# Optimization experiments

Hardware: AMD Instinct MI355X
Metric: run time of the kernel (lower is better)

## Reference

```python
import jax, jax.numpy as jnp
import numpy as np

E = 256  # embed_dim (hardcoded in source module)
H = 4    # n_head
D = E // H
SEQ = 32768


def setup_inputs() -> dict:
    key = jax.random.key(0)
    ks = jax.random.split(key, 5)
    x = jax.random.normal(ks[0], (SEQ, E), dtype=jnp.float32)
    in_proj_weight = jax.random.normal(ks[1], (3 * E, E), dtype=jnp.float32) * (1.0 / np.sqrt(E))
    in_proj_bias = jax.random.normal(ks[2], (3 * E,), dtype=jnp.float32) * 0.02
    out_proj_weight = jax.random.normal(ks[3], (E, E), dtype=jnp.float32) * (1.0 / np.sqrt(E))
    out_proj_bias = jax.random.normal(ks[4], (E,), dtype=jnp.float32) * 0.02
    return {
        "x": x,
        "in_proj_weight": in_proj_weight,
        "in_proj_bias": in_proj_bias,
        "out_proj_weight": out_proj_weight,
        "out_proj_bias": out_proj_bias,
    }


def reference(x, in_proj_weight, in_proj_bias, out_proj_weight, out_proj_bias):
    # QKV projections (q uses only the first token of x: single-query decode attention)
    Wq, Wk, Wv = in_proj_weight[:E], in_proj_weight[E:2 * E], in_proj_weight[2 * E:]
    bq, bk, bv = in_proj_bias[:E], in_proj_bias[E:2 * E], in_proj_bias[2 * E:]
    q = x[:1] @ Wq.T + bq            # [1, E]
    k = x @ Wk.T + bk                # [S, E]
    v = x @ Wv.T + bv                # [S, E]

    qh = q.reshape(H, D)             # [H, D] (single query)
    kh = k.reshape(-1, H, D)         # [S, H, D]
    vh = v.reshape(-1, H, D)         # [S, H, D]

    scale = 1.0 / np.sqrt(D).astype(np.float32)
    scores = jnp.einsum("hd,shd->hs", qh, kh) * scale   # [H, S]
    attn = jax.nn.softmax(scores, axis=-1)                # [H, S]
    ctx = jnp.einsum("hs,shd->hd", attn, vh)             # [H, D]

    out = ctx.reshape(1, E) @ out_proj_weight.T + out_proj_bias  # [1, E]
    return out
```

## Files before the change

kernel.cpp:

```cpp
#include <hip/hip_runtime.h>

#define NBLK 256
#define WS_MP   0
#define WS_LP   1024
#define WS_YV   2048
#define WS_B2   3072
#define WS_KQ   3328
#define WS_C4   4352
#define WS_M2   4416
#define WS_YP   266560
#define WS_CNT  528704

__device__ __forceinline__ float dot4(float4 a, float4 b) {
  return a.x * b.x + a.y * b.y + a.z * b.z + a.w * b.w;
}

__device__ __forceinline__ void set_flag(int* slot, int t) {
  __threadfence();
  __syncthreads();
  if (t == 0) __hip_atomic_store(slot, 1, __ATOMIC_RELEASE, __HIP_MEMORY_SCOPE_AGENT);
}
__device__ __forceinline__ void poll_flags(const int* flags, int n, int t) {
  const int idx = t & (n - 1);
  for (;;) {
    int v = __hip_atomic_load((int*)&flags[idx], __ATOMIC_RELAXED, __HIP_MEMORY_SCOPE_AGENT);
    if (__syncthreads_and(v != 0)) break;
    __builtin_amdgcn_s_sleep(2);
  }
  __threadfence();
}

__device__ __forceinline__ void phaseA_kq(const float* __restrict__ x, const float* __restrict__ W,
                                          const float* __restrict__ inb, float* __restrict__ kq,
                                          float* __restrict__ c4, float* sh, int bid, int t) {
  float* xs = sh;
  float* qls = sh + 256;
  float* red = sh + 320;
  const int lane = t & 63, w = t >> 6;
  const int h = bid >> 2, qt = bid & 3;
  if (t < 256) xs[t] = x[t];
  __syncthreads();
  const float4 xv = *(const float4*)&xs[lane * 4];
#pragma unroll
  for (int k = 0; k < 8; ++k) {
    const int eloc = w * 8 + k;
    const int row = h * 64 + eloc;
    float4 wv = *(const float4*)&W[(size_t)row * 256 + lane * 4];
    float p = dot4(wv, xv);
#pragma unroll
    for (int m = 1; m < 64; m <<= 1) p += __shfl_xor(p, m);
    if (lane == 0) qls[eloc] = p + inb[row];
  }
  __syncthreads();
  const int cl = t & 63, ds = t >> 6;
  float acc = 0.f;
#pragma unroll
  for (int d2 = 0; d2 < 8; ++d2) {
    const int d = ds * 8 + d2;
    acc += W[(size_t)(256 + h * 64 + d) * 256 + qt * 64 + cl] * qls[d];
  }
  red[ds * 64 + cl] = acc;
  __syncthreads();
  if (ds == 0) {
    float s = 0.f;
#pragma unroll
    for (int i = 0; i < 8; ++i) s += red[i * 64 + cl];
    kq[h * 256 + qt * 64 + cl] = s;
  }
  if (qt == 0 && t < 64) {
    float v = qls[t] * inb[256 + h * 64 + t];
#pragma unroll
    for (int m = 1; m < 64; m <<= 1) v += __shfl_xor(v, m);
    if (t == 0) c4[h] = v;
  }
}

__device__ __forceinline__ void phaseM2b(const float* __restrict__ W, const float* __restrict__ Wout,
                                         const float* __restrict__ inb, const float* __restrict__ bout,
                                         float* __restrict__ M2, float* __restrict__ bias2,
                                         float* sh, int b2, int t) {
  float* wout_t = sh;
  const int tile = b2 >> 1, sub = b2 & 1;
  const int h = tile >> 4, e0 = (tile & 15) * 16 + sub * 8;
  {
    const int e = t >> 6, d = t & 63;
    wout_t[e * 64 + d] = Wout[(size_t)(e0 + e) * 256 + h * 64 + d];
  }
  __syncthreads();
  const int c = t & 255, eh = t >> 8;
  float acc[4] = {0.f, 0.f, 0.f, 0.f};
#pragma unroll 8
  for (int d = 0; d < 64; ++d) {
    const float wv = W[(size_t)(512 + h * 64 + d) * 256 + c];
#pragma unroll
    for (int e = 0; e < 4; ++e) acc[e] += wv * wout_t[(eh * 4 + e) * 64 + d];
  }
#pragma unroll
  for (int e = 0; e < 4; ++e)
    M2[(size_t)(e0 + eh * 4 + e) * 1024 + h * 256 + c] = acc[e];
  __syncthreads();
  float* red = sh;
  const int oi = t >> 8, seg = t & 255;
  const int e = 2 * b2 + oi;
  red[oi * 256 + seg] = Wout[(size_t)e * 256 + seg] * inb[512 + seg];
  __syncthreads();
  for (int s = 128; s > 0; s >>= 1) {
    if (seg < s) red[oi * 256 + seg] += red[oi * 256 + seg + s];
    __syncthreads();
  }
  if (t < 2) bias2[2 * b2 + t] = red[t * 256] + bout[2 * b2 + t];
}

__device__ __forceinline__ float bscore(float4 xv, float4 kq0, float4 kq1, float4 kq2,
                                        float4 kq3, float c4v, int lane) {
  float p0 = dot4(xv, kq0), p1 = dot4(xv, kq1), p2 = dot4(xv, kq2), p3 = dot4(xv, kq3);
  const bool b1 = (lane & 2) != 0;
  float keep0 = b1 ? p2 : p0, send0 = b1 ? p0 : p2;
  keep0 += __shfl_xor(send0, 2);
  float keep1 = b1 ? p3 : p1, send1 = b1 ? p1 : p3;
  keep1 += __shfl_xor(send1, 2);
  const bool b0 = (lane & 1) != 0;
  float vv = b0 ? keep1 : keep0, sv = b0 ? keep0 : keep1;
  vv += __shfl_xor(sv, 1);
  vv += __shfl_xor(vv, 4);
  vv += __shfl_xor(vv, 8);
  vv += __shfl_xor(vv, 16);
  vv += __shfl_xor(vv, 32);
  return (vv + c4v) * 0.125f;
}

__device__ __forceinline__ void phaseB_core(const float4* xvA, const float4* xvB,
                                            const float* __restrict__ kq, const float* __restrict__ c4,
                                            float* __restrict__ ypart, float* __restrict__ mpart,
                                            float* __restrict__ lpart, float* yls, int bid, int t) {
  float* sml = yls + 8192;
  float* sll = yls + 8224;
  const int lane = t & 63, w = t >> 6;
  const int hme = lane & 3;
  const float4 kq0 = *(const float4*)&kq[0 * 256 + lane * 4];
  const float4 kq1 = *(const float4*)&kq[1 * 256 + lane * 4];
  const float4 kq2 = *(const float4*)&kq[2 * 256 + lane * 4];
  const float4 kq3 = *(const float4*)&kq[3 * 256 + lane * 4];
  const float c4v = c4[hme];

  float vA[8];
#pragma unroll
  for (int r = 0; r < 8; ++r) vA[r] = bscore(xvA[r], kq0, kq1, kq2, kq3, c4v, lane);
  float m = vA[0];
#pragma unroll
  for (int r = 1; r < 8; ++r) m = fmaxf(m, vA[r]);

  float l = 0.f;
  float4 a[4];
#pragma unroll
  for (int k = 0; k < 4; ++k) a[k] = (float4){0.f, 0.f, 0.f, 0.f};
#pragma unroll
  for (int r = 0; r < 8; ++r) {
    const float e0 = __expf(vA[r] - m);
    l += e0;
    const float e1 = __shfl_xor(e0, 1);
    const float e2 = __shfl_xor(e0, 2);
    const float e3 = __shfl_xor(e0, 3);
    a[0].x += e0 * xvA[r].x; a[0].y += e0 * xvA[r].y; a[0].z += e0 * xvA[r].z; a[0].w += e0 * xvA[r].w;
    a[1].x += e1 * xvA[r].x; a[1].y += e1 * xvA[r].y; a[1].z += e1 * xvA[r].z; a[1].w += e1 * xvA[r].w;
    a[2].x += e2 * xvA[r].x; a[2].y += e2 * xvA[r].y; a[2].z += e2 * xvA[r].z; a[2].w += e2 * xvA[r].w;
    a[3].x += e3 * xvA[r].x; a[3].y += e3 * xvA[r].y; a[3].z += e3 * xvA[r].z; a[3].w += e3 * xvA[r].w;
  }

  float vB[8];
#pragma unroll
  for (int r = 0; r < 8; ++r) vB[r] = bscore(xvB[r], kq0, kq1, kq2, kq3, c4v, lane);
  float mB = vB[0];
#pragma unroll
  for (int r = 1; r < 8; ++r) mB = fmaxf(mB, vB[r]);

  {
    const float mN = fmaxf(m, mB);
    const float fown = __expf(m - mN);
    l *= fown;
    const float f1 = __shfl_xor(fown, 1);
    const float f2 = __shfl_xor(fown, 2);
    const float f3 = __shfl_xor(fown, 3);
    a[0].x *= fown; a[0].y *= fown; a[0].z *= fown; a[0].w *= fown;
    a[1].x *= f1;   a[1].y *= f1;   a[1].z *= f1;   a[1].w *= f1;
    a[2].x *= f2;   a[2].y *= f2;   a[2].z *= f2;   a[2].w *= f2;
    a[3].x *= f3;   a[3].y *= f3;   a[3].z *= f3;   a[3].w *= f3;
    m = mN;
  }
#pragma unroll
  for (int r = 0; r < 8; ++r) {
    const float e0 = __expf(vB[r] - m);
    l += e0;
    const float e1 = __shfl_xor(e0, 1);
    const float e2 = __shfl_xor(e0, 2);
    const float e3 = __shfl_xor(e0, 3);
    a[0].x += e0 * xvB[r].x; a[0].y += e0 * xvB[r].y; a[0].z += e0 * xvB[r].z; a[0].w += e0 * xvB[r].w;
    a[1].x += e1 * xvB[r].x; a[1].y += e1 * xvB[r].y; a[1].z += e1 * xvB[r].z; a[1].w += e1 * xvB[r].w;
    a[2].x += e2 * xvB[r].x; a[2].y += e2 * xvB[r].y; a[2].z += e2 * xvB[r].z; a[2].w += e2 * xvB[r].w;
    a[3].x += e3 * xvB[r].x; a[3].y += e3 * xvB[r].y; a[3].z += e3 * xvB[r].z; a[3].w += e3 * xvB[r].w;
  }

  __syncthreads();
  if (lane < 4) { sml[w * 4 + lane] = m; sll[w * 4 + lane] = l; }
  __syncthreads();

#pragma unroll
  for (int k = 0; k < 4; ++k) {
    const int h = hme ^ k;
    float mb = sml[h];
#pragma unroll
    for (int i = 1; i < 8; ++i) mb = fmaxf(mb, sml[i * 4 + h]);
    const float f = __expf(sml[w * 4 + h] - mb);
    float4 av;
    av.x = a[k].x * f; av.y = a[k].y * f; av.z = a[k].z * f; av.w = a[k].w * f;
    *(float4*)&yls[w * 1024 + h * 256 + lane * 4] = av;
  }
  __syncthreads();

  if (t < 4) {
    float mb = sml[t];
#pragma unroll
    for (int i = 1; i < 8; ++i) mb = fmaxf(mb, sml[i * 4 + t]);
    float lb = 0.f;
#pragma unroll
    for (int i = 0; i < 8; ++i) lb += sll[i * 4 + t] * __expf(sml[i * 4 + t] - mb);
    mpart[t * NBLK + bid] = mb;
    lpart[t * NBLK + bid] = lb;
  }
  float* yp = &ypart[(size_t)bid * 1024];
#pragma unroll
  for (int o = t; o < 1024; o += 512) {
    float s = 0.f;
#pragma unroll
    for (int i = 0; i < 8; ++i) s += yls[i * 1024 + o];
    yp[o] = s;
  }
}

__device__ __forceinline__ void phaseC(const float* __restrict__ ypart, const float* __restrict__ mpart,
                                       const float* __restrict__ lpart, float* __restrict__ yv,
                                       float* sh, int bid, int t) {
  float* mred = sh;
  float* scales = sh + 256;
  float* lred = sh + 512;
  float* sred = sh + 768;
  const int h = bid >> 4;
  const int o0 = bid * 16;
  if (t < 256) mred[t] = mpart[h * 256 + t];
  __syncthreads();
  for (int s = 128; s > 0; s >>= 1) {
    if (t < s) mred[t] = fmaxf(mred[t], mred[t + s]);
    __syncthreads();
  }
  const float mg = mred[0];
  if (t < 256) {
    const float sc = __expf(mpart[h * 256 + t] - mg);
    scales[t] = sc;
    lred[t] = lpart[h * 256 + t] * sc;
  }
  __syncthreads();
  for (int s = 128; s > 0; s >>= 1) {
    if (t < s) lred[t] += lred[t + s];
    __syncthreads();
  }
  const float inv = 1.0f / lred[0];
  const int ol = t & 15, bg = t >> 4;
  float s = 0.f;
#pragma unroll
  for (int j = 0; j < 8; ++j) {
    const int b = bg * 8 + j;
    s += ypart[(size_t)b * 1024 + o0 + ol] * scales[b];
  }
  sred[bg * 16 + ol] = s;
  __syncthreads();
  if (t < 16) {
    float tot = 0.f;
#pragma unroll
    for (int g = 0; g < 32; ++g) tot += sred[g * 16 + t];
    yv[o0 + t] = tot * inv;
  }
}

__device__ __forceinline__ void phaseD4(const float* __restrict__ M2, const float* __restrict__ yv,
                                        const float* __restrict__ bias2, float* __restrict__ out,
                                        float* sh, int bid, int t) {
  float* yls2 = sh;
  float* smo = sh + 1024;
  const int lane = t & 63, w = t >> 6;
  for (int i = t; i < 1024; i += 512) yls2[i] = yv[i];
  __syncthreads();
  const int seg = t & 127;
  const int e = bid * 4 + (t >> 7);
  const float4* m4 = (const float4*)&M2[(size_t)e * 1024];
  const float4* y4 = (const float4*)yls2;
  float acc = dot4(m4[seg * 2], y4[seg * 2]) + dot4(m4[seg * 2 + 1], y4[seg * 2 + 1]);
#pragma unroll
  for (int m = 1; m < 64; m <<= 1) acc += __shfl_xor(acc, m);
  if (lane == 0) smo[w] = acc;
  __syncthreads();
  if (t < 4) out[bid * 4 + t] = smo[2 * t] + smo[2 * t + 1] + bias2[bid * 4 + t];
}

__global__ void __launch_bounds__(512, 1) mha_one(const float* __restrict__ x,
                                                  const float* __restrict__ W,
                                                  const float* __restrict__ inb,
                                                  const float* __restrict__ Wout,
                                                  const float* __restrict__ bout,
                                                  float* __restrict__ out,
                                                  float* __restrict__ ws) {
  __shared__ __align__(16) float sh[8256];
  const int t = threadIdx.x, bid = blockIdx.x;
  const int lane = t & 63, w = t >> 6;
  int* flagA = (int*)(ws + WS_CNT);
  int* flagB = flagA + 16;
  int* flagC = flagB + 256;
  int* flagM = flagC + 64;

  const int r0 = bid * 128 + w * 16;
  float4 xvA[8], xvB[8];

  if (bid >= 16) {
#pragma unroll
    for (int r = 0; r < 8; ++r)
      xvA[r] = *(const float4*)&x[(size_t)(r0 + r) * 256 + lane * 4];
#pragma unroll
    for (int r = 0; r < 8; ++r)
      xvB[r] = *(const float4*)&x[(size_t)(r0 + 8 + r) * 256 + lane * 4];
  } else {
    phaseA_kq(x, W, inb, ws + WS_KQ, ws + WS_C4, sh, bid, t);
    set_flag(&flagA[bid], t);
#pragma unroll
    for (int r = 0; r < 8; ++r)
      xvA[r] = *(const float4*)&x[(size_t)(r0 + r) * 256 + lane * 4];
#pragma unroll
    for (int r = 0; r < 8; ++r)
      xvB[r] = *(const float4*)&x[(size_t)(r0 + 8 + r) * 256 + lane * 4];
  }

  poll_flags(flagA, 16, t);
  phaseB_core(xvA, xvB, ws + WS_KQ, ws + WS_C4, ws + WS_YP, ws + WS_MP, ws + WS_LP, sh, bid, t);
  set_flag(&flagB[bid], t);

  if (bid >= 128) {
    phaseM2b(W, Wout, inb, bout, ws + WS_M2, ws + WS_B2, sh, bid - 128, t);
    set_flag(&flagM[bid - 128], t);
    return;
  }
  if (bid >= 64) return;

  poll_flags(flagB, 256, t);
  phaseC(ws + WS_YP, ws + WS_MP, ws + WS_LP, ws + WS_YV, sh, bid, t);
  set_flag(&flagC[bid], t);
  poll_flags(flagC, 64, t);
  poll_flags(flagM, 128, t);
  phaseD4(ws + WS_M2, ws + WS_YV, ws + WS_B2, out, sh, bid, t);
}

__global__ void __launch_bounds__(512) fb_A(const float* __restrict__ x, const float* __restrict__ W,
                                            const float* __restrict__ inb, float* __restrict__ ws) {
  __shared__ __align__(16) float sh[832];
  phaseA_kq(x, W, inb, ws + WS_KQ, ws + WS_C4, sh, blockIdx.x, threadIdx.x);
}
__global__ void __launch_bounds__(512) fb_B(const float* __restrict__ x, float* __restrict__ ws) {
  __shared__ __align__(16) float sh[8256];
  const int bid = blockIdx.x, t = threadIdx.x;
  const int lane = t & 63, w = t >> 6;
  const int r0 = bid * 128 + w * 16;
  float4 xvA[8], xvB[8];
#pragma unroll
  for (int r = 0; r < 8; ++r)
    xvA[r] = *(const float4*)&x[(size_t)(r0 + r) * 256 + lane * 4];
#pragma unroll
  for (int r = 0; r < 8; ++r)
    xvB[r] = *(const float4*)&x[(size_t)(r0 + 8 + r) * 256 + lane * 4];
  phaseB_core(xvA, xvB, ws + WS_KQ, ws + WS_C4, ws + WS_YP, ws + WS_MP, ws + WS_LP, sh, bid, t);
}
__global__ void __launch_bounds__(512) fb_CM(const float* __restrict__ W, const float* __restrict__ Wout,
                                             const float* __restrict__ inb, const float* __restrict__ bout,
                                             float* __restrict__ ws) {
  __shared__ __align__(16) float sh[1280];
  const int bid = blockIdx.x, t = threadIdx.x;
  if (bid < 64) phaseC(ws + WS_YP, ws + WS_MP, ws + WS_LP, ws + WS_YV, sh, bid, t);
  else phaseM2b(W, Wout, inb, bout, ws + WS_M2, ws + WS_B2, sh, bid - 64, t);
}
__global__ void __launch_bounds__(512) fb_D(float* __restrict__ out, float* __restrict__ ws) {
  __shared__ __align__(16) float sh[1056];
  phaseD4(ws + WS_M2, ws + WS_YV, ws + WS_B2, out, sh, blockIdx.x, threadIdx.x);
}

extern "C" void kernel_launch(void* const* d_in, const int* in_sizes, int n_in,
                              void* d_out, int out_size, void* d_ws, size_t ws_size,
                              hipStream_t stream) {
  const float* x = (const float*)d_in[0];
  const float* W = (const float*)d_in[1];
  const float* inb = (const float*)d_in[2];
  const float* Wout = (const float*)d_in[3];
  const float* bout = (const float*)d_in[4];
  float* out = (float*)d_out;
  float* ws = (float*)d_ws;

  hipMemsetAsync((void*)(ws + WS_CNT), 0, 2048, stream);

  int dev = 0;
  (void)hipGetDevice(&dev);
  int coopAttr = 0, ncu = 0, occ = 0;
  bool coop = (hipDeviceGetAttribute(&coopAttr, hipDeviceAttributeCooperativeLaunch, dev) == hipSuccess) &&
              coopAttr != 0;
  coop = coop &&
         (hipDeviceGetAttribute(&ncu, hipDeviceAttributeMultiprocessorCount, dev) == hipSuccess);
  coop = coop &&
         (hipOccupancyMaxActiveBlocksPerMultiprocessor(&occ, mha_one, 512, 0) == hipSuccess);
  coop = coop && (occ * ncu >= NBLK);

  if (coop) {
    void* args[] = {(void*)&x, (void*)&W, (void*)&inb, (void*)&Wout,
                    (void*)&bout, (void*)&out, (void*)&ws};
    if (hipLaunchCooperativeKernel((const void*)mha_one, dim3(NBLK), dim3(512),
                                   args, 0, stream) == hipSuccess)
      return;
  }
  fb_A<<<16, 512, 0, stream>>>(x, W, inb, ws);
  fb_B<<<NBLK, 512, 0, stream>>>(x, ws);
  fb_CM<<<192, 512, 0, stream>>>(W, Wout, inb, bout, ws);
  fb_D<<<64, 512, 0, stream>>>(out, ws);
}
```

Baseline: 36.05 us.

## Replace fused M2 precompute with staged ctx and output projections, use grid sync

```diff
diff --git a/kernel.cpp b/kernel.cpp
--- a/kernel.cpp
+++ b/kernel.cpp
@@ -1,15 +1,16 @@
 #include <hip/hip_runtime.h>
+#include <hip/hip_cooperative_groups.h>
+namespace cg = cooperative_groups;
 
 #define NBLK 256
 #define WS_MP   0
 #define WS_LP   1024
 #define WS_YV   2048
-#define WS_B2   3072
+#define WS_CTX  3072
 #define WS_KQ   3328
 #define WS_C4   4352
-#define WS_M2   4416
-#define WS_YP   266560
-#define WS_CNT  528704
+#define WS_YP   4416
+#define WS_CNT  266560
 
 __device__ __forceinline__ float dot4(float4 a, float4 b) {
   return a.x * b.x + a.y * b.y + a.z * b.z + a.w * b.w;
@@ -73,42 +74,6 @@
     for (int m = 1; m < 64; m <<= 1) v += __shfl_xor(v, m);
     if (t == 0) c4[h] = v;
   }
-}
-
-__device__ __forceinline__ void phaseM2b(const float* __restrict__ W, const float* __restrict__ Wout,
-                                         const float* __restrict__ inb, const float* __restrict__ bout,
-                                         float* __restrict__ M2, float* __restrict__ bias2,
-                                         float* sh, int b2, int t) {
-  float* wout_t = sh;
-  const int tile = b2 >> 1, sub = b2 & 1;
-  const int h = tile >> 4, e0 = (tile & 15) * 16 + sub * 8;
-  {
-    const int e = t >> 6, d = t & 63;
-    wout_t[e * 64 + d] = Wout[(size_t)(e0 + e) * 256 + h * 64 + d];
-  }
-  __syncthreads();
-  const int c = t & 255, eh = t >> 8;
-  float acc[4] = {0.f, 0.f, 0.f, 0.f};
-#pragma unroll 8
-  for (int d = 0; d < 64; ++d) {
-    const float wv = W[(size_t)(512 + h * 64 + d) * 256 + c];
-#pragma unroll
-    for (int e = 0; e < 4; ++e) acc[e] += wv * wout_t[(eh * 4 + e) * 64 + d];
-  }
-#pragma unroll
-  for (int e = 0; e < 4; ++e)
-    M2[(size_t)(e0 + eh * 4 + e) * 1024 + h * 256 + c] = acc[e];
-  __syncthreads();
-  float* red = sh;
-  const int oi = t >> 8, seg = t & 255;
-  const int e = 2 * b2 + oi;
-  red[oi * 256 + seg] = Wout[(size_t)e * 256 + seg] * inb[512 + seg];
-  __syncthreads();
-  for (int s = 128; s > 0; s >>= 1) {
-    if (seg < s) red[oi * 256 + seg] += red[oi * 256 + seg + s];
-    __syncthreads();
-  }
-  if (t < 2) bias2[2 * b2 + t] = red[t * 256] + bout[2 * b2 + t];
 }
 
 __device__ __forceinline__ float bscore(float4 xv, float4 kq0, float4 kq1, float4 kq2,
@@ -143,12 +108,17 @@
   const float4 kq3 = *(const float4*)&kq[3 * 256 + lane * 4];
   const float c4v = c4[hme];
 
-  float vA[8];
+  float vA[8], vB[8];
 #pragma unroll
   for (int r = 0; r < 8; ++r) vA[r] = bscore(xvA[r], kq0, kq1, kq2, kq3, c4v, lane);
+#pragma unroll
+  for (int r = 0; r < 8; ++r) vB[r] = bscore(xvB[r], kq0, kq1, kq2, kq3, c4v, lane);
+
   float m = vA[0];
 #pragma unroll
   for (int r = 1; r < 8; ++r) m = fmaxf(m, vA[r]);
+#pragma unroll
+  for (int r = 0; r < 8; ++r) m = fmaxf(m, vB[r]);
 
   float l = 0.f;
   float4 a[4];
@@ -166,27 +136,6 @@
     a[2].x += e2 * xvA[r].x; a[2].y += e2 * xvA[r].y; a[2].z += e2 * xvA[r].z; a[2].w += e2 * xvA[r].w;
     a[3].x += e3 * xvA[r].x; a[3].y += e3 * xvA[r].y; a[3].z += e3 * xvA[r].z; a[3].w += e3 * xvA[r].w;
   }
-
-  float vB[8];
-#pragma unroll
-  for (int r = 0; r < 8; ++r) vB[r] = bscore(xvB[r], kq0, kq1, kq2, kq3, c4v, lane);
-  float mB = vB[0];
-#pragma unroll
-  for (int r = 1; r < 8; ++r) mB = fmaxf(mB, vB[r]);
-
-  {
-    const float mN = fmaxf(m, mB);
-    const float fown = __expf(m - mN);
-    l *= fown;
-    const float f1 = __shfl_xor(fown, 1);
-    const float f2 = __shfl_xor(fown, 2);
-    const float f3 = __shfl_xor(fown, 3);
-    a[0].x *= fown; a[0].y *= fown; a[0].z *= fown; a[0].w *= fown;
-    a[1].x *= f1;   a[1].y *= f1;   a[1].z *= f1;   a[1].w *= f1;
-    a[2].x *= f2;   a[2].y *= f2;   a[2].z *= f2;   a[2].w *= f2;
-    a[3].x *= f3;   a[3].y *= f3;   a[3].z *= f3;   a[3].w *= f3;
-    m = mN;
-  }
 #pragma unroll
   for (int r = 0; r < 8; ++r) {
     const float e0 = __expf(vB[r] - m);
@@ -281,24 +230,36 @@
   }
 }
 
-__device__ __forceinline__ void phaseD4(const float* __restrict__ M2, const float* __restrict__ yv,
-                                        const float* __restrict__ bias2, float* __restrict__ out,
-                                        float* sh, int bid, int t) {
-  float* yls2 = sh;
-  float* smo = sh + 1024;
-  const int lane = t & 63, w = t >> 6;
-  for (int i = t; i < 1024; i += 512) yls2[i] = yv[i];
-  __syncthreads();
-  const int seg = t & 127;
-  const int e = bid * 4 + (t >> 7);
-  const float4* m4 = (const float4*)&M2[(size_t)e * 1024];
-  const float4* y4 = (const float4*)yls2;
-  float acc = dot4(m4[seg * 2], y4[seg * 2]) + dot4(m4[seg * 2 + 1], y4[seg * 2 + 1]);
-#pragma unroll
-  for (int m = 1; m < 64; m <<= 1) acc += __shfl_xor(acc, m);
-  if (lane == 0) smo[w] = acc;
-  __syncthreads();
-  if (t < 4) out[bid * 4 + t] = smo[2 * t] + smo[2 * t + 1] + bias2[bid * 4 + t];
+__device__ __forceinline__ void phaseCtx(const float* __restrict__ W, const float* __restrict__ inb,
+                                         const float* __restrict__ yv, float* __restrict__ ctx,
+                                         int b, int t) {
+  const int lane = t & 63, w = t >> 6;
+  if (w < 4) {
+    const int i = b * 4 + w;
+    const int h = i >> 6;
+    float4 wv = *(const float4*)&W[(size_t)(512 + i) * 256 + lane * 4];
+    float4 yy = *(const float4*)&yv[h * 256 + lane * 4];
+    float p = dot4(wv, yy);
+#pragma unroll
+    for (int m = 1; m < 64; m <<= 1) p += __shfl_xor(p, m);
+    if (lane == 0) ctx[i] = p + inb[512 + i];
+  }
+}
+
+__device__ __forceinline__ void phaseOut(const float* __restrict__ Wout, const float* __restrict__ bout,
+                                         const float* __restrict__ ctx, float* __restrict__ out,
+                                         int b, int t) {
+  const int lane = t & 63, w = t >> 6;
+  const float4 cv = *(const float4*)&ctx[lane * 4];
+#pragma unroll
+  for (int k = 0; k < 2; ++k) {
+    const int e = b * 16 + w * 2 + k;
+    float4 wv = *(const float4*)&Wout[(size_t)e * 256 + lane * 4];
+    float p = dot4(wv, cv);
+#pragma unroll
+    for (int m = 1; m < 64; m <<= 1) p += __shfl_xor(p, m);
+    if (lane == 0) out[e] = p + bout[e];
+  }
 }
 
 __global__ void __launch_bounds__(512, 1) mha_one(const float* __restrict__ x,
@@ -312,14 +273,16 @@
   const int t = threadIdx.x, bid = blockIdx.x;
   const int lane = t & 63, w = t >> 6;
   int* flagA = (int*)(ws + WS_CNT);
-  int* flagB = flagA + 16;
-  int* flagC = flagB + 256;
-  int* flagM = flagC + 64;
+  int* flagC = flagA + 16;
+  int* flagX = flagC + 64;
+  cg::grid_group grid = cg::this_grid();
 
   const int r0 = bid * 128 + w * 16;
   float4 xvA[8], xvB[8];
 
-  if (bid >= 16) {
+  if (bid < 16) {
+    phaseA_kq(x, W, inb, ws + WS_KQ, ws + WS_C4, sh, bid, t);
+    set_flag(&flagA[bid], t);
 #pragma unroll
     for (int r = 0; r < 8; ++r)
       xvA[r] = *(const float4*)&x[(size_t)(r0 + r) * 256 + lane * 4];
@@ -327,8 +290,6 @@
     for (int r = 0; r < 8; ++r)
       xvB[r] = *(const float4*)&x[(size_t)(r0 + 8 + r) * 256 + lane * 4];
   } else {
-    phaseA_kq(x, W, inb, ws + WS_KQ, ws + WS_C4, sh, bid, t);
-    set_flag(&flagA[bid], t);
 #pragma unroll
     for (int r = 0; r < 8; ++r)
       xvA[r] = *(const float4*)&x[(size_t)(r0 + r) * 256 + lane * 4];
@@ -339,21 +300,20 @@
 
   poll_flags(flagA, 16, t);
   phaseB_core(xvA, xvB, ws + WS_KQ, ws + WS_C4, ws + WS_YP, ws + WS_MP, ws + WS_LP, sh, bid, t);
-  set_flag(&flagB[bid], t);
-
-  if (bid >= 128) {
-    phaseM2b(W, Wout, inb, bout, ws + WS_M2, ws + WS_B2, sh, bid - 128, t);
-    set_flag(&flagM[bid - 128], t);
-    return;
-  }
-  if (bid >= 64) return;
-
-  poll_flags(flagB, 256, t);
-  phaseC(ws + WS_YP, ws + WS_MP, ws + WS_LP, ws + WS_YV, sh, bid, t);
-  set_flag(&flagC[bid], t);
-  poll_flags(flagC, 64, t);
-  poll_flags(flagM, 128, t);
-  phaseD4(ws + WS_M2, ws + WS_YV, ws + WS_B2, out, sh, bid, t);
+
+  grid.sync();
+
+  if (bid < 64) {
+    phaseC(ws + WS_YP, ws + WS_MP, ws + WS_LP, ws + WS_YV, sh, bid, t);
+    set_flag(&flagC[bid], t);
+  } else if (bid < 128) {
+    poll_flags(flagC, 64, t);
+    phaseCtx(W, inb, ws + WS_YV, ws + WS_CTX, bid - 64, t);
+    set_flag(&flagX[bid - 64], t);
+  } else if (bid < 144) {
+    poll_flags(flagX, 64, t);
+    phaseOut(Wout, bout, ws + WS_CTX, out, bid - 128, t);
+  }
 }
 
 __global__ void __launch_bounds__(512) fb_A(const float* __restrict__ x, const float* __restrict__ W,
@@ -375,17 +335,17 @@
     xvB[r] = *(const float4*)&x[(size_t)(r0 + 8 + r) * 256 + lane * 4];
   phaseB_core(xvA, xvB, ws + WS_KQ, ws + WS_C4, ws + WS_YP, ws + WS_MP, ws + WS_LP, sh, bid, t);
 }
-__global__ void __launch_bounds__(512) fb_CM(const float* __restrict__ W, const float* __restrict__ Wout,
-                                             const float* __restrict__ inb, const float* __restrict__ bout,
-                                             float* __restrict__ ws) {
+__global__ void __launch_bounds__(512) fb_C(float* __restrict__ ws) {
   __shared__ __align__(16) float sh[1280];
-  const int bid = blockIdx.x, t = threadIdx.x;
-  if (bid < 64) phaseC(ws + WS_YP, ws + WS_MP, ws + WS_LP, ws + WS_YV, sh, bid, t);
-  else phaseM2b(W, Wout, inb, bout, ws + WS_M2, ws + WS_B2, sh, bid - 64, t);
-}
-__global__ void __launch_bounds__(512) fb_D(float* __restrict__ out, float* __restrict__ ws) {
-  __shared__ __align__(16) float sh[1056];
-  phaseD4(ws + WS_M2, ws + WS_YV, ws + WS_B2, out, sh, blockIdx.x, threadIdx.x);
+  phaseC(ws + WS_YP, ws + WS_MP, ws + WS_LP, ws + WS_YV, sh, blockIdx.x, threadIdx.x);
+}
+__global__ void __launch_bounds__(512) fb_X(const float* __restrict__ W, const float* __restrict__ inb,
+                                            float* __restrict__ ws) {
+  phaseCtx(W, inb, ws + WS_YV, ws + WS_CTX, blockIdx.x, threadIdx.x);
+}
+__global__ void __launch_bounds__(512) fb_O(const float* __restrict__ Wout, const float* __restrict__ bout,
+                                            float* __restrict__ out, float* __restrict__ ws) {
+  phaseOut(Wout, bout, ws + WS_CTX, out, blockIdx.x, threadIdx.x);
 }
 
 extern "C" void kernel_launch(void* const* d_in, const int* in_sizes, int n_in,
@@ -399,7 +359,7 @@
   float* out = (float*)d_out;
   float* ws = (float*)d_ws;
 
-  hipMemsetAsync((void*)(ws + WS_CNT), 0, 2048, stream);
+  hipMemsetAsync((void*)(ws + WS_CNT), 0, 1024, stream);
 
   int dev = 0;
   (void)hipGetDevice(&dev);
@@ -421,6 +381,7 @@
   }
   fb_A<<<16, 512, 0, stream>>>(x, W, inb, ws);
   fb_B<<<NBLK, 512, 0, stream>>>(x, ws);
-  fb_CM<<<192, 512, 0, stream>>>(W, Wout, inb, bout, ws);
-  fb_D<<<64, 512, 0, stream>>>(out, ws);
-}
+  fb_C<<<64, 512, 0, stream>>>(ws);
+  fb_X<<<64, 512, 0, stream>>>(W, inb, ws);
+  fb_O<<<16, 512, 0, stream>>>(Wout, bout, out, ws);
+}
```

Result: no change. 35.90 us (-0.4%).
